# Kernel tuning notes

Hardware: AMD Instinct MI355X
Metric: run time of the kernel (lower is better)

The kernel has to match this reference:

```python
import jax, jax.numpy as jnp
import numpy as np
from jax import lax

B, C, H, W = 8, 512, 64, 64
K = 3            # dynamic depthwise kernel size
GROUPS = C       # n_groups defaults to in_channels (depthwise)
EPS = 1e-5


def setup_inputs() -> dict:
    key = jax.random.key(0)
    ks = jax.random.split(key, 6)
    x = jax.random.normal(ks[0], (B, C, H, W), dtype=jnp.float32)
    w_spatial = jax.random.normal(ks[1], (B, C, 1, K, K), dtype=jnp.float32) * 0.05
    w_pointwise = jax.random.normal(ks[2], (B, C, 1, 1, 1), dtype=jnp.float32) * 0.05
    bias = jax.random.normal(ks[3], (B, C), dtype=jnp.float32) * 0.05
    # shared final conv (nn.Conv2d(C, C, 3, reflect pad, bias=True))
    conv_w = jax.random.normal(ks[4], (C, C, 3, 3), dtype=jnp.float32) * 0.02
    conv_b = jax.random.normal(ks[5], (C,), dtype=jnp.float32) * 0.02
    return {"x": x, "w_spatial": w_spatial, "w_pointwise": w_pointwise,
            "bias": bias, "conv_w": conv_w, "conv_b": conv_b}


def _instance_norm(x):
    # F.instance_norm defaults: no affine, biased variance, eps=1e-5
    mu = jnp.mean(x, axis=(2, 3), keepdims=True)
    var = jnp.var(x, axis=(2, 3), keepdims=True)
    return (x - mu) * lax.rsqrt(var + EPS)


def _reflect_pad(x, p):
    return jnp.pad(x, ((0, 0), (0, 0), (p, p), (p, p)), mode="reflect")


def _conv(x, w, groups):
    return lax.conv_general_dilated(
        x, w, window_strides=(1, 1), padding="VALID",
        feature_group_count=groups,
        dimension_numbers=("NCHW", "OIHW", "NCHW"))


def _forward_single(xn, ws, wp, b):
    # xn: [C,H,W]; ws: [C,1,K,K]; wp: [C,1,1,1]; b: [C]
    p = (ws.shape[-1] - 1) // 2
    xp = _reflect_pad(xn[None], p)            # [1,C,H+2p,W+2p]
    y = _conv(xp, ws, GROUPS)                 # depthwise spatial conv
    y = _conv(y, wp, GROUPS)                  # grouped pointwise conv
    return (y + b[None, :, None, None])[0]    # [C,H,W]


def reference(x, w_spatial, w_pointwise, bias, conv_w, conv_b):
    xn = _instance_norm(x)
    mid = jax.vmap(_forward_single)(xn, w_spatial, w_pointwise, bias)  # [B,C,H,W]
    out = _conv(_reflect_pad(mid, 1), conv_w, 1) + conv_b[None, :, None, None]
    return out
```

## Files before the change

### kernel.cpp

```cpp
#include <hip/hip_runtime.h>
#include <hip/hip_bf16.h>


#define EPSV 1e-5f

typedef __attribute__((ext_vector_type(8))) short short8;
typedef __attribute__((ext_vector_type(4))) float f32x4;

template<int N> struct IC { static constexpr int value = N; };

__device__ __forceinline__ unsigned short f2bf(float f) {
  union { float f; unsigned int u; } v; v.f = f;
  unsigned int r = v.u + 0x7FFFu + ((v.u >> 16) & 1u);
  return (unsigned short)(r >> 16);
}

__device__ __forceinline__ int refl(int i, int n) {
  if (i < 0) i = -i;
  if (i >= n) i = 2 * n - 2 - i;
  return i;
}

__global__ __launch_bounds__(256) void k_stats(const float* __restrict__ x,
                                               float* __restrict__ mean,
                                               float* __restrict__ rstd) {
  int bc = blockIdx.x;
  const float4* xp = (const float4*)(x + (size_t)bc * 4096);
  int tid = threadIdx.x;
  float s = 0.f, q = 0.f;
#pragma unroll
  for (int k = 0; k < 4; ++k) {
    float4 v = xp[tid + k * 256];
    s += v.x + v.y + v.z + v.w;
    q += v.x * v.x + v.y * v.y + v.z * v.z + v.w * v.w;
  }
  __shared__ float s1[256], s2[256];
  s1[tid] = s; s2[tid] = q;
  __syncthreads();
  for (int st = 128; st > 0; st >>= 1) {
    if (tid < st) { s1[tid] += s1[tid + st]; s2[tid] += s2[tid + st]; }
    __syncthreads();
  }
  if (tid == 0) {
    float m = s1[0] * (1.f / 4096.f);
    float var = s2[0] * (1.f / 4096.f) - m * m;
    mean[bc] = m;
    rstd[bc] = rsqrtf(var + EPSV);
  }
}

__global__ __launch_bounds__(256) void k_wprep(const float* __restrict__ cw,
                                               unsigned short* __restrict__ wT2) {
  int idx = blockIdx.x * 256 + threadIdx.x;
  int e = idx & 7;
  int l15 = (idx >> 3) & 15;
  int g = (idx >> 7) & 3;
  int cq = (idx >> 9) & 15;
  int og = (idx >> 13) & 31;
  int t = idx >> 18;
  int o = og * 16 + l15;
  int c = cq * 32 + g * 8 + e;
  wT2[idx] = f2bf(cw[((size_t)(o * 512 + c)) * 9 + t]);
}

__global__ __launch_bounds__(256) void k_mid(const float* __restrict__ x,
                                             const float* __restrict__ wsp,
                                             const float* __restrict__ wpw,
                                             const float* __restrict__ bias,
                                             const float* __restrict__ mean,
                                             const float* __restrict__ rstd,
                                             unsigned short* __restrict__ mid) {
  int bid = blockIdx.x;
  int cg = bid & 3;
  int hq = (bid >> 2) & 15;
  int b = bid >> 6;
  int h0 = hq * 4;
  int tid = threadIdx.x;
  int cl = tid & 31, wq = tid >> 5;
  __shared__ float xs[32 * 391];

  int rowm[6];
#pragma unroll
  for (int r = 0; r < 6; ++r) rowm[r] = refl(h0 - 1 + r, 64);

  for (int cc = 0; cc < 4; ++cc) {
    int cbase = cg * 128 + cc * 32;
    __syncthreads();
#pragma unroll
    for (int k = 0; k < 12; ++k) {
      int idx = tid + k * 256;
      int c = idx / 96, rem = idx % 96;
      int r = rem >> 4, w4 = rem & 15;
      float4 v = *(const float4*)(x + ((size_t)(b * 512 + cbase + c)) * 4096 +
                                  rowm[r] * 64 + w4 * 4);
      float* dst = &xs[c * 391 + r * 65 + w4 * 4];
      dst[0] = v.x; dst[1] = v.y; dst[2] = v.z; dst[3] = v.w;
    }
    __syncthreads();

    int gc = b * 512 + cbase + cl;
    float m = mean[gc], rs = rstd[gc];
    float wp = wpw[gc], bv = bias[gc];
    float wk[9], wsum = 0.f;
#pragma unroll
    for (int t = 0; t < 9; ++t) { wk[t] = wsp[(size_t)gc * 9 + t]; wsum += wk[t]; }

    const float* xr = &xs[cl * 391];
#pragma unroll
    for (int r = 0; r < 4; ++r) {
#pragma unroll
      for (int wi = 0; wi < 8; ++wi) {
        int w = wq * 8 + wi;
        int wm = refl(w - 1, 64), wp1 = refl(w + 1, 64);
        float acc = 0.f;
#pragma unroll
        for (int dy = 0; dy < 3; ++dy) {
          const float* row = xr + (r + dy) * 65;
          acc += wk[dy * 3 + 0] * row[wm] + wk[dy * 3 + 1] * row[w] +
                 wk[dy * 3 + 2] * row[wp1];
        }
        float y = (acc - m * wsum) * rs;
        mid[(((size_t)(b * 64 + h0 + r)) * 64 + w) * 512 + cbase + cl] =
            f2bf(y * wp + bv);
      }
    }
  }
}

__global__ __launch_bounds__(512, 2) void k_conv(const unsigned short* __restrict__ wT2,
                                                 const unsigned short* __restrict__ mid,
                                                 const float* __restrict__ cb,
                                                 float* __restrict__ out) {
  int nbid = (blockIdx.x & 7) * 32 + (blockIdx.x >> 3);
  int mt = nbid >> 7;
  int b = (nbid >> 4) & 7;
  int h0 = (nbid & 15) * 4;
  int tid = threadIdx.x;
  int wid = tid >> 6, l = tid & 63;
  int wo = wid & 3, wn = wid >> 2;
  int l15 = l & 15, g = l >> 4;

  __shared__ union {
    unsigned short bbuf[2][6 * 64 * 32];
    float epi[64 * 132];
  } sm;

  int hrow_[6];
#pragma unroll
  for (int r = 0; r < 6; ++r) hrow_[r] = refl(h0 - 1 + r, 64);

  int boff[4][3];
#pragma unroll
  for (int ww = 0; ww < 4; ++ww)
#pragma unroll
    for (int dx = 0; dx < 3; ++dx) {
      int wr = refl(ww * 16 + l15 + dx - 1, 64);
      int s = g ^ ((wr >> 1) & 3);
      boff[ww][dx] = wr * 64 + s * 16;
    }

  f32x4 acc[4][8];
  f32x4 zero = {0.f, 0.f, 0.f, 0.f};
#pragma unroll
  for (int i = 0; i < 4; ++i)
#pragma unroll
    for (int j = 0; j < 8; ++j) acc[i][j] = zero;

  auto stageB = [&](int pi, int cc) {
    int cb32 = cc * 32;
    char* dstbase = (char*)&sm.bbuf[pi][0];
#pragma unroll
    for (int i = 0; i < 3; ++i) {
      int ld = tid + i * 512;
      int row = ld >> 8, rem = ld & 255, w = rem >> 2, s = rem & 3;
      int gcg = s ^ ((w >> 1) & 3);
      const unsigned short* src = mid +
          (((size_t)(b * 64 + hrow_[row])) * 64 + w) * 512 + cb32 + gcg * 8;
      __builtin_amdgcn_global_load_lds(
          (const __attribute__((address_space(1))) void*)src,
          (__attribute__((address_space(3))) void*)(dstbase + ld * 16),
          16, 0, 0);
    }
  };

  stageB(0, 0);

  const unsigned short* wa0 =
      wT2 + ((size_t)((mt * 16 + wo * 4) * 16)) * 512 + l * 8;

  short8 aC[4];
  {
    const unsigned short* wp0 = wa0 + (size_t)(wn * 4) * 262144;
#pragma unroll
    for (int of = 0; of < 4; ++of)
      aC[of] = *(const short8*)(wp0 + of * 8192);
  }

  for (int cc = 0; cc < 16; ++cc) {
    int pb = cc & 1;
    __syncthreads();
    if (cc < 15) stageB(pb ^ 1, cc + 1);
    const char* mb = (const char*)&sm.bbuf[pb][0];

    auto taps = [&](auto rotc) {
      constexpr int ROT = decltype(rotc)::value;
#pragma unroll
      for (int t = 0; t < 9; ++t) {
        const int tr = (t + ROT) % 9;
        const int dy = tr / 3, dx = tr % 3;

        const int trn = (t + 1 + ROT) % 9;
        const int ccn = (t < 8) ? cc : ((cc + 1) & 15);
        const unsigned short* wan =
            wa0 + (size_t)trn * 262144 + (size_t)ccn * 512;
        short8 aN[4];
#pragma unroll
        for (int of = 0; of < 4; ++of)
          aN[of] = *(const short8*)(wan + of * 8192);

        __builtin_amdgcn_s_setprio(1);
#pragma unroll
        for (int nf = 0; nf < 8; ++nf) {
          const int rowL = wn * 2 + (nf >> 2) + dy;
          short8 bf = *(const short8*)(mb + rowL * 4096 + boff[nf & 3][dx]);
#pragma unroll
          for (int of = 0; of < 4; ++of)
            acc[of][nf] = __builtin_amdgcn_mfma_f32_16x16x32_bf16(
                aC[of], bf, acc[of][nf], 0, 0, 0);
        }
        __builtin_amdgcn_s_setprio(0);
#pragma unroll
        for (int of = 0; of < 4; ++of) aC[of] = aN[of];
      }
    };
    if (wn == 0) taps(IC<0>{});
    else         taps(IC<4>{});
  }

#pragma unroll
  for (int p = 0; p < 4; ++p)
#pragma unroll
    for (int s = 0; s < 2; ++s) {
      __syncthreads();
      if (wo == p && wn == s) {
#pragma unroll
        for (int of = 0; of < 4; ++of)
#pragma unroll
          for (int nf = 0; nf < 8; ++nf) {
            int pix = (nf >> 2) * 64 + (nf & 3) * 16 + l15;
#pragma unroll
            for (int r = 0; r < 4; ++r) {
              int ol = of * 16 + g * 4 + r;
              sm.epi[ol * 132 + pix] = acc[of][nf][r];
            }
          }
      }
      __syncthreads();
#pragma unroll
      for (int it = 0; it < 4; ++it) {
        int idx = tid + it * 512;
        int ol = idx >> 5, rem = idx & 31;
        f32x4 v = *(const f32x4*)&sm.epi[ol * 132 + rem * 4];
        int o = mt * 256 + p * 64 + ol;
        float cbv = cb[o];
        v[0] += cbv; v[1] += cbv; v[2] += cbv; v[3] += cbv;
        int pix = rem * 4;
        int hh = h0 + s * 2 + (pix >> 6);
        int w4 = pix & 63;
        *(f32x4*)(out + (((size_t)(b * 512 + o)) * 64 + hh) * 64 + w4) = v;
      }
    }
}

extern "C" void kernel_launch(void* const* d_in, const int* in_sizes, int n_in,
                              void* d_out, int out_size, void* d_ws, size_t ws_size,
                              hipStream_t stream) {
  const float* x    = (const float*)d_in[0];
  const float* wsp  = (const float*)d_in[1];
  const float* wpw  = (const float*)d_in[2];
  const float* bias = (const float*)d_in[3];
  const float* cw   = (const float*)d_in[4];
  const float* cb   = (const float*)d_in[5];
  float* out = (float*)d_out;

  char* ws = (char*)d_ws;
  float* mean = (float*)ws;
  float* rstd = (float*)(ws + 16384);
  unsigned short* wT2 = (unsigned short*)(ws + 32768);
  unsigned short* mid = (unsigned short*)(ws + 32768 + 9 * 512 * 512 * 2);

  k_stats<<<4096, 256, 0, stream>>>(x, mean, rstd);
  k_wprep<<<9216, 256, 0, stream>>>(cw, wT2);
  k_mid<<<512, 256, 0, stream>>>(x, wsp, wpw, bias, mean, rstd, mid);
  k_conv<<<256, 512, 0, stream>>>(wT2, mid, cb, out);
}
```

Before: 172.1 us.

## Switch main conv to 32x32x16 bf16 MFMA with new weight/LDS layout

```diff
diff --git a/kernel.cpp b/kernel.cpp
--- a/kernel.cpp
+++ b/kernel.cpp
@@ -6,6 +6,7 @@
 
 typedef __attribute__((ext_vector_type(8))) short short8;
 typedef __attribute__((ext_vector_type(4))) float f32x4;
+typedef __attribute__((ext_vector_type(16))) float f32x16;
 
 template<int N> struct IC { static constexpr int value = N; };
 
@@ -50,17 +51,16 @@
 }
 
 __global__ __launch_bounds__(256) void k_wprep(const float* __restrict__ cw,
-                                               unsigned short* __restrict__ wT2) {
+                                               unsigned short* __restrict__ wT3) {
   int idx = blockIdx.x * 256 + threadIdx.x;
   int e = idx & 7;
-  int l15 = (idx >> 3) & 15;
-  int g = (idx >> 7) & 3;
-  int cq = (idx >> 9) & 15;
-  int og = (idx >> 13) & 31;
+  int l = (idx >> 3) & 63;
+  int c16 = (idx >> 9) & 31;
+  int ot = (idx >> 14) & 15;
   int t = idx >> 18;
-  int o = og * 16 + l15;
-  int c = cq * 32 + g * 8 + e;
-  wT2[idx] = f2bf(cw[((size_t)(o * 512 + c)) * 9 + t]);
+  int o = ot * 32 + (l & 31);
+  int c = c16 * 16 + (l >> 5) * 8 + e;
+  wT3[idx] = f2bf(cw[((size_t)(o * 512 + c)) * 9 + t]);
 }
 
 __global__ __launch_bounds__(256) void k_mid(const float* __restrict__ x,
@@ -127,7 +127,7 @@
   }
 }
 
-__global__ __launch_bounds__(512, 2) void k_conv(const unsigned short* __restrict__ wT2,
+__global__ __launch_bounds__(512, 2) void k_conv(const unsigned short* __restrict__ wT3,
                                                  const unsigned short* __restrict__ mid,
                                                  const float* __restrict__ cb,
                                                  float* __restrict__ out) {
@@ -138,10 +138,11 @@
   int tid = threadIdx.x;
   int wid = tid >> 6, l = tid & 63;
   int wo = wid & 3, wn = wid >> 2;
-  int l15 = l & 15, g = l >> 4;
+  int l31 = l & 31;
+  int lso = (l >> 5) * 1024;
 
   __shared__ union {
-    unsigned short bbuf[2][6 * 64 * 32];
+    unsigned short bbuf[2][6 * 4 * 64 * 8];
     float epi[64 * 132];
   } sm;
 
@@ -149,33 +150,29 @@
 #pragma unroll
   for (int r = 0; r < 6; ++r) hrow_[r] = refl(h0 - 1 + r, 64);
 
-  int boff[4][3];
-#pragma unroll
-  for (int ww = 0; ww < 4; ++ww)
-#pragma unroll
-    for (int dx = 0; dx < 3; ++dx) {
-      int wr = refl(ww * 16 + l15 + dx - 1, 64);
-      int s = g ^ ((wr >> 1) & 3);
-      boff[ww][dx] = wr * 64 + s * 16;
-    }
-
-  f32x4 acc[4][8];
-  f32x4 zero = {0.f, 0.f, 0.f, 0.f};
-#pragma unroll
-  for (int i = 0; i < 4; ++i)
-#pragma unroll
-    for (int j = 0; j < 8; ++j) acc[i][j] = zero;
+  int wrv2[2][3];
+#pragma unroll
+  for (int i = 0; i < 2; ++i)
+#pragma unroll
+    for (int dx = 0; dx < 3; ++dx)
+      wrv2[i][dx] = refl(i * 32 + l31 + dx - 1, 64) * 16;
+
+  f32x16 acc[2][4];
+#pragma unroll
+  for (int i = 0; i < 2; ++i)
+#pragma unroll
+    for (int j = 0; j < 4; ++j)
+#pragma unroll
+      for (int r = 0; r < 16; ++r) acc[i][j][r] = 0.f;
 
   auto stageB = [&](int pi, int cc) {
-    int cb32 = cc * 32;
     char* dstbase = (char*)&sm.bbuf[pi][0];
 #pragma unroll
     for (int i = 0; i < 3; ++i) {
       int ld = tid + i * 512;
-      int row = ld >> 8, rem = ld & 255, w = rem >> 2, s = rem & 3;
-      int gcg = s ^ ((w >> 1) & 3);
+      int row = ld >> 8, rem = ld & 255, slot = rem >> 6, w = rem & 63;
       const unsigned short* src = mid +
-          (((size_t)(b * 64 + hrow_[row])) * 64 + w) * 512 + cb32 + gcg * 8;
+          (((size_t)(b * 64 + hrow_[row])) * 64 + w) * 512 + cc * 32 + slot * 8;
       __builtin_amdgcn_global_load_lds(
           (const __attribute__((address_space(1))) void*)src,
           (__attribute__((address_space(3))) void*)(dstbase + ld * 16),
@@ -186,14 +183,16 @@
   stageB(0, 0);
 
   const unsigned short* wa0 =
-      wT2 + ((size_t)((mt * 16 + wo * 4) * 16)) * 512 + l * 8;
+      wT3 + ((size_t)((mt * 8 + wo * 2) * 32)) * 512 + l * 8;
 
   short8 aC[4];
   {
     const unsigned short* wp0 = wa0 + (size_t)(wn * 4) * 262144;
 #pragma unroll
-    for (int of = 0; of < 4; ++of)
-      aC[of] = *(const short8*)(wp0 + of * 8192);
+    for (int kh = 0; kh < 2; ++kh)
+#pragma unroll
+      for (int ot = 0; ot < 2; ++ot)
+        aC[kh * 2 + ot] = *(const short8*)(wp0 + ot * 16384 + kh * 512);
   }
 
   for (int cc = 0; cc < 16; ++cc) {
@@ -204,33 +203,51 @@
 
     auto taps = [&](auto rotc) {
       constexpr int ROT = decltype(rotc)::value;
+      const int dy0 = (ROT % 9) / 3, dx0 = (ROT % 9) % 3;
+      short8 bfC = *(const short8*)(mb + (wn * 2 + dy0) * 4096 + lso + wrv2[0][dx0]);
 #pragma unroll
       for (int t = 0; t < 9; ++t) {
         const int tr = (t + ROT) % 9;
         const int dy = tr / 3, dx = tr % 3;
 
         const int trn = (t + 1 + ROT) % 9;
+        const int dyn = trn / 3, dxn = trn % 3;
         const int ccn = (t < 8) ? cc : ((cc + 1) & 15);
-        const unsigned short* wan =
-            wa0 + (size_t)trn * 262144 + (size_t)ccn * 512;
+        const unsigned short* wan = wa0 + (size_t)trn * 262144;
         short8 aN[4];
 #pragma unroll
-        for (int of = 0; of < 4; ++of)
-          aN[of] = *(const short8*)(wan + of * 8192);
+        for (int kh = 0; kh < 2; ++kh)
+#pragma unroll
+          for (int ot = 0; ot < 2; ++ot)
+            aN[kh * 2 + ot] =
+                *(const short8*)(wan + ot * 16384 + (size_t)(ccn * 2 + kh) * 512);
 
         __builtin_amdgcn_s_setprio(1);
 #pragma unroll
-        for (int nf = 0; nf < 8; ++nf) {
-          const int rowL = wn * 2 + (nf >> 2) + dy;
-          short8 bf = *(const short8*)(mb + rowL * 4096 + boff[nf & 3][dx]);
-#pragma unroll
-          for (int of = 0; of < 4; ++of)
-            acc[of][nf] = __builtin_amdgcn_mfma_f32_16x16x32_bf16(
-                aC[of], bf, acc[of][nf], 0, 0, 0);
-        }
+        for (int kh = 0; kh < 2; ++kh)
+#pragma unroll
+          for (int pt = 0; pt < 4; ++pt) {
+            const int f = kh * 4 + pt;
+            short8 bfN;
+            if (f < 7) {
+              const int khn = (f + 1) >> 2, ptn = (f + 1) & 3;
+              bfN = *(const short8*)(mb + (wn * 2 + (ptn >> 1) + dy) * 4096 +
+                                     khn * 2048 + lso + wrv2[ptn & 1][dx]);
+            } else if (t < 8) {
+              bfN = *(const short8*)(mb + (wn * 2 + dyn) * 4096 +
+                                     lso + wrv2[0][dxn]);
+            } else {
+              bfN = bfC;
+            }
+#pragma unroll
+            for (int ot = 0; ot < 2; ++ot)
+              acc[ot][pt] = __builtin_amdgcn_mfma_f32_32x32x16_bf16(
+                  aC[kh * 2 + ot], bfC, acc[ot][pt], 0, 0, 0);
+            bfC = bfN;
+          }
         __builtin_amdgcn_s_setprio(0);
 #pragma unroll
-        for (int of = 0; of < 4; ++of) aC[of] = aN[of];
+        for (int i = 0; i < 4; ++i) aC[i] = aN[i];
       }
     };
     if (wn == 0) taps(IC<0>{});
@@ -244,14 +261,14 @@
       __syncthreads();
       if (wo == p && wn == s) {
 #pragma unroll
-        for (int of = 0; of < 4; ++of)
-#pragma unroll
-          for (int nf = 0; nf < 8; ++nf) {
-            int pix = (nf >> 2) * 64 + (nf & 3) * 16 + l15;
-#pragma unroll
-            for (int r = 0; r < 4; ++r) {
-              int ol = of * 16 + g * 4 + r;
-              sm.epi[ol * 132 + pix] = acc[of][nf][r];
+        for (int ot = 0; ot < 2; ++ot)
+#pragma unroll
+          for (int pt = 0; pt < 4; ++pt) {
+            int pix = (pt >> 1) * 64 + (pt & 1) * 32 + l31;
+#pragma unroll
+            for (int reg = 0; reg < 16; ++reg) {
+              int ol = ot * 32 + (reg & 3) + 8 * (reg >> 2) + 4 * (l >> 5);
+              sm.epi[ol * 132 + pix] = acc[ot][pt][reg];
             }
           }
       }
@@ -286,11 +303,11 @@
   char* ws = (char*)d_ws;
   float* mean = (float*)ws;
   float* rstd = (float*)(ws + 16384);
-  unsigned short* wT2 = (unsigned short*)(ws + 32768);
+  unsigned short* wT3 = (unsigned short*)(ws + 32768);
   unsigned short* mid = (unsigned short*)(ws + 32768 + 9 * 512 * 512 * 2);
 
   k_stats<<<4096, 256, 0, stream>>>(x, mean, rstd);
-  k_wprep<<<9216, 256, 0, stream>>>(cw, wT2);
+  k_wprep<<<9216, 256, 0, stream>>>(cw, wT3);
   k_mid<<<512, 256, 0, stream>>>(x, wsp, wpw, bias, mean, rstd, mid);
-  k_conv<<<256, 512, 0, stream>>>(wT2, mid, cb, out);
-}
+  k_conv<<<256, 512, 0, stream>>>(wT3, mid, cb, out);
+}
```

Measured after the change: 178.6 us. +3.7%, slower.

## Remap conv warp tiling to 2x4 with 128 output channels per wave

Applied to the files above, without the earlier changes.

```diff
diff --git a/kernel.cpp b/kernel.cpp
--- a/kernel.cpp
+++ b/kernel.cpp
@@ -137,12 +137,12 @@
   int h0 = (nbid & 15) * 4;
   int tid = threadIdx.x;
   int wid = tid >> 6, l = tid & 63;
-  int wo = wid & 3, wn = wid >> 2;
+  int wo = wid >> 2, wn = wid & 3;
   int l15 = l & 15, g = l >> 4;
 
   __shared__ union {
     unsigned short bbuf[2][6 * 64 * 32];
-    float epi[64 * 132];
+    float epi[64 * 260];
   } sm;
 
   int hrow_[6];
@@ -159,12 +159,12 @@
       boff[ww][dx] = wr * 64 + s * 16;
     }
 
-  f32x4 acc[4][8];
+  f32x4 acc[8][4];
   f32x4 zero = {0.f, 0.f, 0.f, 0.f};
 #pragma unroll
-  for (int i = 0; i < 4; ++i)
-#pragma unroll
-    for (int j = 0; j < 8; ++j) acc[i][j] = zero;
+  for (int i = 0; i < 8; ++i)
+#pragma unroll
+    for (int j = 0; j < 4; ++j) acc[i][j] = zero;
 
   auto stageB = [&](int pi, int cc) {
     int cb32 = cc * 32;
@@ -186,13 +186,13 @@
   stageB(0, 0);
 
   const unsigned short* wa0 =
-      wT2 + ((size_t)((mt * 16 + wo * 4) * 16)) * 512 + l * 8;
-
-  short8 aC[4];
+      wT2 + ((size_t)((mt * 16 + wo * 8) * 16)) * 512 + l * 8;
+
+  short8 aC[8];
   {
-    const unsigned short* wp0 = wa0 + (size_t)(wn * 4) * 262144;
-#pragma unroll
-    for (int of = 0; of < 4; ++of)
+    const unsigned short* wp0 = wa0 + (size_t)(wo * 4) * 262144;
+#pragma unroll
+    for (int of = 0; of < 8; ++of)
       aC[of] = *(const short8*)(wp0 + of * 8192);
   }
 
@@ -208,68 +208,69 @@
       for (int t = 0; t < 9; ++t) {
         const int tr = (t + ROT) % 9;
         const int dy = tr / 3, dx = tr % 3;
+        const int rowL = wn + dy;
+
+        short8 bf[4];
+#pragma unroll
+        for (int nf = 0; nf < 4; ++nf)
+          bf[nf] = *(const short8*)(mb + rowL * 4096 + boff[nf][dx]);
 
         const int trn = (t + 1 + ROT) % 9;
         const int ccn = (t < 8) ? cc : ((cc + 1) & 15);
         const unsigned short* wan =
             wa0 + (size_t)trn * 262144 + (size_t)ccn * 512;
-        short8 aN[4];
-#pragma unroll
-        for (int of = 0; of < 4; ++of)
+        short8 aN[8];
+#pragma unroll
+        for (int of = 0; of < 8; ++of)
           aN[of] = *(const short8*)(wan + of * 8192);
 
         __builtin_amdgcn_s_setprio(1);
 #pragma unroll
-        for (int nf = 0; nf < 8; ++nf) {
-          const int rowL = wn * 2 + (nf >> 2) + dy;
-          short8 bf = *(const short8*)(mb + rowL * 4096 + boff[nf & 3][dx]);
-#pragma unroll
-          for (int of = 0; of < 4; ++of)
+        for (int nf = 0; nf < 4; ++nf)
+#pragma unroll
+          for (int of = 0; of < 8; ++of)
             acc[of][nf] = __builtin_amdgcn_mfma_f32_16x16x32_bf16(
-                aC[of], bf, acc[of][nf], 0, 0, 0);
-        }
+                aC[of], bf[nf], acc[of][nf], 0, 0, 0);
         __builtin_amdgcn_s_setprio(0);
 #pragma unroll
-        for (int of = 0; of < 4; ++of) aC[of] = aN[of];
+        for (int of = 0; of < 8; ++of) aC[of] = aN[of];
       }
     };
-    if (wn == 0) taps(IC<0>{});
+    if (wo == 0) taps(IC<0>{});
     else         taps(IC<4>{});
   }
 
 #pragma unroll
-  for (int p = 0; p < 4; ++p)
-#pragma unroll
-    for (int s = 0; s < 2; ++s) {
-      __syncthreads();
-      if (wo == p && wn == s) {
-#pragma unroll
-        for (int of = 0; of < 4; ++of)
-#pragma unroll
-          for (int nf = 0; nf < 8; ++nf) {
-            int pix = (nf >> 2) * 64 + (nf & 3) * 16 + l15;
-#pragma unroll
-            for (int r = 0; r < 4; ++r) {
-              int ol = of * 16 + g * 4 + r;
-              sm.epi[ol * 132 + pix] = acc[of][nf][r];
-            }
+  for (int p = 0; p < 4; ++p) {
+    __syncthreads();
+    if (wo == (p >> 1)) {
+      const int ofb = (p & 1) * 4;
+#pragma unroll
+      for (int ofl = 0; ofl < 4; ++ofl)
+#pragma unroll
+        for (int nf = 0; nf < 4; ++nf) {
+          int pix = wn * 64 + nf * 16 + l15;
+#pragma unroll
+          for (int r = 0; r < 4; ++r) {
+            int ol = ofl * 16 + g * 4 + r;
+            sm.epi[ol * 260 + pix] = acc[ofb + ofl][nf][r];
           }
-      }
-      __syncthreads();
-#pragma unroll
-      for (int it = 0; it < 4; ++it) {
-        int idx = tid + it * 512;
-        int ol = idx >> 5, rem = idx & 31;
-        f32x4 v = *(const f32x4*)&sm.epi[ol * 132 + rem * 4];
-        int o = mt * 256 + p * 64 + ol;
-        float cbv = cb[o];
-        v[0] += cbv; v[1] += cbv; v[2] += cbv; v[3] += cbv;
-        int pix = rem * 4;
-        int hh = h0 + s * 2 + (pix >> 6);
-        int w4 = pix & 63;
-        *(f32x4*)(out + (((size_t)(b * 512 + o)) * 64 + hh) * 64 + w4) = v;
-      }
-    }
+        }
+    }
+    __syncthreads();
+#pragma unroll
+    for (int it = 0; it < 8; ++it) {
+      int idx = tid + it * 512;
+      int ol = idx >> 6, rem = idx & 63;
+      f32x4 v = *(const f32x4*)&sm.epi[ol * 260 + rem * 4];
+      int o = mt * 256 + p * 64 + ol;
+      float cbv = cb[o];
+      v[0] += cbv; v[1] += cbv; v[2] += cbv; v[3] += cbv;
+      int hh = h0 + (rem >> 4);
+      int w4 = (rem & 15) * 4;
+      *(f32x4*)(out + (((size_t)(b * 512 + o)) * 64 + hh) * 64 + w4) = v;
+    }
+  }
 }
 
 extern "C" void kernel_launch(void* const* d_in, const int* in_sizes, int n_in,
```

Measured after the change: 183.6 us. 6.7% more time.
